# Kernel optimization log

Hardware: AMD Instinct MI355X
Metric: run time of the kernel (lower is better)

## Reference

```python
import jax, jax.numpy as jnp
import numpy as np
from jax import lax

FS, DW, CIN, COUT, NCLS, BATCH = 128, 8, 64, 256, 2, 512
K1, S1 = FS // 4, FS // 8          # 32, 16
L = FS * DW                        # 1024
T = (L - K1) // S1 + 1             # 63 SNN timesteps
BN_EPS = 1e-5


@jax.custom_vjp
def spike(u):
    """Heaviside spike on (v - threshold); surrogate grad exp(-|u|) (tau_grad=scale_grad=1)."""
    return (u >= 0).astype(u.dtype)

def _spike_fwd(u):
    return (u >= 0).astype(u.dtype), u

def _spike_bwd(u, g):
    return (g * jnp.exp(-jnp.abs(u)),)

spike.defvjp(_spike_fwd, _spike_bwd)


def cuba(x, threshold, current_decay, voltage_decay):
    """CUBA LIF scan. x: [N,C,T] -> binary spikes [N,C,T].
    i[t] = (1-cd)*i[t-1] + x[t]; v[t] = (1-vd)*v[t-1] + i[t]; s = v>=theta; v *= (1-s)."""
    cd, vd = 1.0 - current_decay, 1.0 - voltage_decay
    xs = jnp.moveaxis(x, -1, 0)  # [T,N,C]
    zero = jnp.zeros(x.shape[:-1], x.dtype)

    def step(carry, xt):
        i, v = carry
        i = cd * i + xt
        v = vd * v + i
        s = spike(v - threshold)
        v = v * (1.0 - s)
        return (i, v), s

    _, s = lax.scan(step, (zero, zero), xs)
    return jnp.moveaxis(s, 0, -1)


def conv1d(x, w, b, stride, pad):
    y = lax.conv_general_dilated(x, w, (stride,), [(pad, pad)],
                                 dimension_numbers=('NCH', 'OIH', 'NCH'))
    return y + b[None, :, None]


def bn(x, g, b, m, v):
    scale = g / jnp.sqrt(v + BN_EPS)
    return (x - m[None, :, None]) * scale[None, :, None] + b[None, :, None]


def setup_inputs() -> dict:
    key = jax.random.key(0)
    ks = jax.random.split(key, 12)
    return {
        'x':       jax.random.normal(ks[0], (BATCH, CIN, L), jnp.float32),
        'conv1_w': jax.random.normal(ks[1], (COUT, CIN, K1), jnp.float32) * 0.05,
        'conv1_b': jax.random.normal(ks[2], (COUT,), jnp.float32) * 0.05,
        'bn1_g':   jax.random.uniform(ks[3], (COUT,), jnp.float32, 0.5, 1.5),
        'bn1_b':   jax.random.normal(ks[4], (COUT,), jnp.float32) * 0.1,
        'bn1_m':   jax.random.normal(ks[5], (COUT,), jnp.float32) * 0.1,
        'bn1_v':   jax.random.uniform(ks[6], (COUT,), jnp.float32, 0.5, 1.5),
        'conv2_w': jax.random.normal(ks[7], (COUT, COUT, 3), jnp.float32) * 0.05,
        'conv2_b': jax.random.normal(ks[8], (COUT,), jnp.float32) * 0.05,
        'bn2_g':   jax.random.uniform(ks[9], (COUT,), jnp.float32, 0.5, 1.5),
        'bn2_b':   jax.random.normal(ks[10], (COUT,), jnp.float32) * 0.1,
        'bn2_m':   jax.random.normal(ks[11], (COUT,), jnp.float32) * 0.1,
        'bn2_v':   jax.random.uniform(jax.random.fold_in(key, 100), (COUT,), jnp.float32, 0.5, 1.5),
        'w1':      jax.random.normal(jax.random.fold_in(key, 101), (COUT, COUT), jnp.float32) * 0.1,
        'w2':      jax.random.normal(jax.random.fold_in(key, 102), (NCLS, COUT), jnp.float32) * 0.1,
    }


def reference(x, conv1_w, conv1_b, bn1_g, bn1_b, bn1_m, bn1_v,
              conv2_w, conv2_b, bn2_g, bn2_b, bn2_m, bn2_v, w1, w2):
    # CNN frontend (eval mode: BN uses running stats, dropout is identity)
    z = bn(conv1d(x, conv1_w, conv1_b, S1, 0), bn1_g, bn1_b, bn1_m, bn1_v)   # [N,COUT,T]
    z = bn(conv1d(z, conv2_w, conv2_b, 1, 1), bn2_g, bn2_b, bn2_m, bn2_v)    # [N,COUT,T]
    # CUBA Input encoder block: threshold=0.3, current_decay=0.9, voltage_decay=0.9
    z = cuba(z, 0.3, 0.9, 0.9)
    # CUBA Dense blocks (bias-free synapse per timestep + LIF): threshold=0.1, cd=1, vd=0.1
    z = cuba(jnp.einsum('oc,nct->not', w1, z), 0.1, 1.0, 0.1)
    z = cuba(jnp.einsum('oc,nct->not', w2, z), 0.1, 1.0, 0.1)
    return z  # binary spike trains [N, n_classes, T]
```

## Files before the change

### kernel.cpp

```cpp
#include <hip/hip_runtime.h>
#include <cstdint>
#include <cstddef>


typedef _Float16 half8 __attribute__((ext_vector_type(8)));
typedef float floatx4 __attribute__((ext_vector_type(4)));

__device__ __forceinline__ void split_f32(float v, _Float16& hi, _Float16& lo) {
    _Float16 h = (_Float16)v;
    hi = h;
    lo = (_Float16)((v - (float)h) * 2048.0f);
}

typedef const __attribute__((address_space(1))) unsigned int* gas_ptr;
typedef __attribute__((address_space(3))) unsigned int* las_ptr;
__device__ __forceinline__ void lds_dma16(const void* g, void* l) {
    __builtin_amdgcn_global_load_lds((gas_ptr)g, (las_ptr)l, 16, 0, 0);
}

__global__ __launch_bounds__(256) void prep_kernel(
    const float* __restrict__ c1w, const float* __restrict__ c1b,
    const float* __restrict__ g1,  const float* __restrict__ b1,
    const float* __restrict__ m1,  const float* __restrict__ v1,
    const float* __restrict__ c2w, const float* __restrict__ c2b,
    const float* __restrict__ g2,  const float* __restrict__ b2,
    const float* __restrict__ m2,  const float* __restrict__ v2,
    const float* __restrict__ w1,
    _Float16* __restrict__ w1h, _Float16* __restrict__ w1l,
    _Float16* __restrict__ w2h, _Float16* __restrict__ w2l,
    _Float16* __restrict__ wdh, _Float16* __restrict__ wdl,
    _Float16* __restrict__ z1ph, _Float16* __restrict__ z1pl,
    float* __restrict__ ab1, float* __restrict__ ab2)
{
    const int id = blockIdx.x * 256 + threadIdx.x;
    if (id < 256) {
        float a1 = g1[id] / sqrtf(v1[id] + 1e-5f);
        ab1[id]       = a1;
        ab1[256 + id] = (c1b[id] - m1[id]) * a1 + b1[id];
        float a2 = g2[id] / sqrtf(v2[id] + 1e-5f);
        ab2[id]       = a2;
        ab2[256 + id] = (c2b[id] - m2[id]) * a2 + b2[id];
    }
    {
        const int n  = id >> 7;
        const int j  = id & 127;
        const int row = (j < 64) ? 0 : 64;
        const int c0  = (j & 63) * 4;
        const size_t off = ((size_t)n * 65 + row) * 256 + c0;
        short4 zz = {0, 0, 0, 0};
        *(short4*)&z1ph[off] = zz;
        *(short4*)&z1pl[off] = zz;
    }
    split_f32(w1[id], wdh[id], wdl[id]);
    for (int idx = id; idx < 256 * 2048; idx += 65536)
        split_f32(c1w[idx], w1h[idx], w1l[idx]);
    for (int idx = id; idx < 256 * 768; idx += 65536) {
        const int o  = idx / 768;
        const int r  = idx - o * 768;
        const int dt = r >> 8;
        const int c  = r & 255;
        split_f32(c2w[o * 768 + c * 3 + dt], w2h[idx], w2l[idx]);
    }
}

__global__ __launch_bounds__(256, 2) void conv1_mfma(
    const float* __restrict__ x,
    const _Float16* __restrict__ w1h, const _Float16* __restrict__ w1l,
    const float* __restrict__ ab,
    _Float16* __restrict__ z1ph, _Float16* __restrict__ z1pl)
{
    __shared__ _Float16 Ah[4][128][8];
    __shared__ _Float16 Al[4][128][8];
    __shared__ _Float16 Bh[4][128][8];
    __shared__ _Float16 Bl[4][128][8];

    const int tid = threadIdx.x;
    const int bm = blockIdx.x, bn = blockIdx.y;
    const int lr = tid & 127;
    const int h  = tid >> 7;

    const int am = bm * 128 + lr;
    const int an = am / 63, at = am - an * 63;
    const float*    arow  = x   + (size_t)an * 65536 + at * 16 + h * 16;
    const _Float16* bhrow = w1h + (size_t)(bn * 128 + lr) * 2048 + h * 16;
    const _Float16* blrow = w1l + (size_t)(bn * 128 + lr) * 2048 + h * 16;

    const int lane = tid & 63;
    const int wv   = tid >> 6;
    const int mw   = wv & 1, nw = wv >> 1;
    const int quad = lane >> 4;
    const int l15  = lane & 15;

    floatx4 accA[4][4] = {};
    floatx4 accB[4][4] = {};

    for (int it = 0; it < 64; ++it) {
        const float* ap = arow + it * 1024;
        float va[16];
        *(float4*)&va[0]  = *(const float4*)(ap);
        *(float4*)&va[4]  = *(const float4*)(ap + 4);
        *(float4*)&va[8]  = *(const float4*)(ap + 8);
        *(float4*)&va[12] = *(const float4*)(ap + 12);
        int4 bh0 = *(const int4*)(bhrow + it * 32);
        int4 bh1 = *(const int4*)(bhrow + it * 32 + 8);
        int4 bl0 = *(const int4*)(blrow + it * 32);
        int4 bl1 = *(const int4*)(blrow + it * 32 + 8);

        union U { _Float16 hf[8]; int4 v; };
        U c0h, c0l, c1h, c1l;
#pragma unroll
        for (int j = 0; j < 8; ++j) split_f32(va[j],     c0h.hf[j], c0l.hf[j]);
#pragma unroll
        for (int j = 0; j < 8; ++j) split_f32(va[8 + j], c1h.hf[j], c1l.hf[j]);

        __syncthreads();
        *(int4*)&Ah[2*h  ][lr][0] = c0h.v;
        *(int4*)&Ah[2*h+1][lr][0] = c1h.v;
        *(int4*)&Al[2*h  ][lr][0] = c0l.v;
        *(int4*)&Al[2*h+1][lr][0] = c1l.v;
        *(int4*)&Bh[2*h  ][lr][0] = bh0;
        *(int4*)&Bh[2*h+1][lr][0] = bh1;
        *(int4*)&Bl[2*h  ][lr][0] = bl0;
        *(int4*)&Bl[2*h+1][lr][0] = bl1;
        __syncthreads();

        half8 fah[4], fal[4], fbh[4], fbl[4];
#pragma unroll
        for (int t = 0; t < 4; ++t) {
            fah[t] = *(const half8*)&Ah[quad][mw*64 + t*16 + l15][0];
            fal[t] = *(const half8*)&Al[quad][mw*64 + t*16 + l15][0];
            fbh[t] = *(const half8*)&Bh[quad][nw*64 + t*16 + l15][0];
            fbl[t] = *(const half8*)&Bl[quad][nw*64 + t*16 + l15][0];
        }
#pragma unroll
        for (int ti = 0; ti < 4; ++ti)
#pragma unroll
            for (int tj = 0; tj < 4; ++tj) {
                accA[ti][tj] = __builtin_amdgcn_mfma_f32_16x16x32_f16(fah[ti], fbh[tj], accA[ti][tj], 0, 0, 0);
                accB[ti][tj] = __builtin_amdgcn_mfma_f32_16x16x32_f16(fah[ti], fbl[tj], accB[ti][tj], 0, 0, 0);
                accB[ti][tj] = __builtin_amdgcn_mfma_f32_16x16x32_f16(fal[ti], fbh[tj], accB[ti][tj], 0, 0, 0);
            }
    }

#pragma unroll
    for (int tj = 0; tj < 4; ++tj) {
        const int o = bn*128 + nw*64 + tj*16 + l15;
        const float alpha = ab[o], beta = ab[256 + o];
#pragma unroll
        for (int ti = 0; ti < 4; ++ti) {
            const int m0 = bm*128 + mw*64 + ti*16 + quad*4;
#pragma unroll
            for (int r = 0; r < 4; ++r) {
                float c = accA[ti][tj][r] + accB[ti][tj][r] * (1.0f/2048.0f);
                float z = c * alpha + beta;
                _Float16 zh, zl;
                split_f32(z, zh, zl);
                const int m  = m0 + r;
                const int a2 = m / 63;
                const int t2 = m - a2 * 63;
                const size_t off = ((size_t)a2 * 65 + t2 + 1) * 256 + o;
                z1ph[off] = zh;
                z1pl[off] = zl;
            }
        }
    }
}

__global__ __launch_bounds__(256, 2) void conv2_mfma(
    const _Float16* __restrict__ z1ph, const _Float16* __restrict__ z1pl,
    const _Float16* __restrict__ w2h, const _Float16* __restrict__ w2l,
    const float* __restrict__ ab, float* __restrict__ z2)
{
    __shared__ _Float16 Ah[8][128][8];
    __shared__ _Float16 Al[8][128][8];
    __shared__ _Float16 Bh[8][128][8];
    __shared__ _Float16 Bl[8][128][8];

    const int tid = threadIdx.x;
    const int bm = blockIdx.x, bn = blockIdx.y;
    const int lr = tid & 127;
    const int h  = tid >> 7;

    const int am = bm * 128 + lr;
    const int an = am / 63, at = am - an * 63;
    const _Float16* pAh = z1ph + (size_t)an * 16640 + at * 256 + h * 8;
    const _Float16* pAl = z1pl + (size_t)an * 16640 + at * 256 + h * 8;
    const _Float16* pBh = w2h + (size_t)(bn * 128 + lr) * 768 + h * 8;
    const _Float16* pBl = w2l + (size_t)(bn * 128 + lr) * 768 + h * 8;

    const int lane = tid & 63;
    const int wv   = tid >> 6;
    const int mw   = wv & 1, nw = wv >> 1;
    const int quad = lane >> 4;
    const int l15  = lane & 15;

    floatx4 accA[4][4] = {};
    floatx4 accB[4][4] = {};

    for (int it = 0; it < 12; ++it) {
        __syncthreads();
#pragma unroll
        for (int q = 0; q < 4; ++q) {
            lds_dma16(pAh + q * 16, &Ah[q*2 + h][lr][0]);
            lds_dma16(pAl + q * 16, &Al[q*2 + h][lr][0]);
            lds_dma16(pBh + q * 16, &Bh[q*2 + h][lr][0]);
            lds_dma16(pBl + q * 16, &Bl[q*2 + h][lr][0]);
        }
        __syncthreads();

#pragma unroll
        for (int ks = 0; ks < 2; ++ks) {
            half8 fah[4], fal[4], fbh[4], fbl[4];
#pragma unroll
            for (int t = 0; t < 4; ++t) {
                fah[t] = *(const half8*)&Ah[ks*4 + quad][mw*64 + t*16 + l15][0];
                fal[t] = *(const half8*)&Al[ks*4 + quad][mw*64 + t*16 + l15][0];
                fbh[t] = *(const half8*)&Bh[ks*4 + quad][nw*64 + t*16 + l15][0];
                fbl[t] = *(const half8*)&Bl[ks*4 + quad][nw*64 + t*16 + l15][0];
            }
#pragma unroll
            for (int ti = 0; ti < 4; ++ti)
#pragma unroll
                for (int tj = 0; tj < 4; ++tj) {
                    accA[ti][tj] = __builtin_amdgcn_mfma_f32_16x16x32_f16(fah[ti], fbh[tj], accA[ti][tj], 0, 0, 0);
                    accB[ti][tj] = __builtin_amdgcn_mfma_f32_16x16x32_f16(fah[ti], fbl[tj], accB[ti][tj], 0, 0, 0);
                    accB[ti][tj] = __builtin_amdgcn_mfma_f32_16x16x32_f16(fal[ti], fbh[tj], accB[ti][tj], 0, 0, 0);
                }
        }
        pAh += 64; pAl += 64; pBh += 64; pBl += 64;
    }

#pragma unroll
    for (int tj = 0; tj < 4; ++tj) {
        const int o = bn*128 + nw*64 + tj*16 + l15;
        const float alpha = ab[o], beta = ab[256 + o];
#pragma unroll
        for (int ti = 0; ti < 4; ++ti) {
            const int m0 = bm*128 + mw*64 + ti*16 + quad*4;
#pragma unroll
            for (int r = 0; r < 4; ++r) {
                float c = accA[ti][tj][r] + accB[ti][tj][r] * (1.0f/2048.0f);
                z2[(size_t)(m0 + r) * 256 + o] = c * alpha + beta;
            }
        }
    }
}

__global__ __launch_bounds__(256) void cuba1_kernel(
    const float* __restrict__ z2, _Float16* __restrict__ s1)
{
    const int n   = blockIdx.x;
    const int tid = threadIdx.x;
    const float* zrow = z2 + (size_t)n * 16128 + tid;
    _Float16*    srow = s1 + (size_t)n * 16128 + tid;
    float cur = 0.f, vol = 0.f;
    for (int tb = 0; tb < 63; tb += 9) {
        float xv[9];
#pragma unroll
        for (int j = 0; j < 9; ++j)
            xv[j] = zrow[(size_t)(tb + j) * 256];
#pragma unroll
        for (int j = 0; j < 9; ++j) {
            cur = 0.1f * cur + xv[j];
            vol = 0.1f * vol + cur;
            bool sp = (vol - 0.3f) >= 0.f;
            srow[(size_t)(tb + j) * 256] = sp ? (_Float16)1.0f : (_Float16)0.0f;
            if (sp) vol = 0.f;
        }
    }
}

__global__ __launch_bounds__(256, 2) void dense1_mfma(
    const _Float16* __restrict__ s1,
    const _Float16* __restrict__ wdh, const _Float16* __restrict__ wdl,
    float* __restrict__ y1)
{
    __shared__ _Float16 As[8][128][8];
    __shared__ _Float16 Bh[8][128][8];
    __shared__ _Float16 Bl[8][128][8];

    const int tid = threadIdx.x;
    const int bm = blockIdx.x, bn = blockIdx.y;
    const int lr = tid & 127;
    const int h  = tid >> 7;

    const _Float16* pA  = s1  + (size_t)(bm * 128 + lr) * 256 + h * 8;
    const _Float16* pBh = wdh + (size_t)(bn * 128 + lr) * 256 + h * 8;
    const _Float16* pBl = wdl + (size_t)(bn * 128 + lr) * 256 + h * 8;

    const int lane = tid & 63;
    const int wv   = tid >> 6;
    const int mw   = wv & 1, nw = wv >> 1;
    const int quad = lane >> 4;
    const int l15  = lane & 15;

    floatx4 accA[4][4] = {};
    floatx4 accB[4][4] = {};

    for (int it = 0; it < 4; ++it) {
        __syncthreads();
#pragma unroll
        for (int q = 0; q < 4; ++q) {
            lds_dma16(pA  + q * 16, &As[q*2 + h][lr][0]);
            lds_dma16(pBh + q * 16, &Bh[q*2 + h][lr][0]);
            lds_dma16(pBl + q * 16, &Bl[q*2 + h][lr][0]);
        }
        __syncthreads();

#pragma unroll
        for (int ks = 0; ks < 2; ++ks) {
            half8 fa[4], fbh[4], fbl[4];
#pragma unroll
            for (int t = 0; t < 4; ++t) {
                fa[t]  = *(const half8*)&As[ks*4 + quad][mw*64 + t*16 + l15][0];
                fbh[t] = *(const half8*)&Bh[ks*4 + quad][nw*64 + t*16 + l15][0];
                fbl[t] = *(const half8*)&Bl[ks*4 + quad][nw*64 + t*16 + l15][0];
            }
#pragma unroll
            for (int ti = 0; ti < 4; ++ti)
#pragma unroll
                for (int tj = 0; tj < 4; ++tj) {
                    accA[ti][tj] = __builtin_amdgcn_mfma_f32_16x16x32_f16(fa[ti], fbh[tj], accA[ti][tj], 0, 0, 0);
                    accB[ti][tj] = __builtin_amdgcn_mfma_f32_16x16x32_f16(fa[ti], fbl[tj], accB[ti][tj], 0, 0, 0);
                }
        }
        pA += 64; pBh += 64; pBl += 64;
    }

#pragma unroll
    for (int tj = 0; tj < 4; ++tj) {
        const int o = bn*128 + nw*64 + tj*16 + l15;
#pragma unroll
        for (int ti = 0; ti < 4; ++ti) {
            const int m0 = bm*128 + mw*64 + ti*16 + quad*4;
#pragma unroll
            for (int r = 0; r < 4; ++r)
                y1[(size_t)(m0 + r) * 256 + o] =
                    accA[ti][tj][r] + accB[ti][tj][r] * (1.0f/2048.0f);
        }
    }
}

__global__ __launch_bounds__(256) void snn_tail(
    const float* __restrict__ y1, const float* __restrict__ w2,
    float* __restrict__ out)
{
    __shared__ unsigned long long M2[256];
    __shared__ float Y[2 * 63];
    const int n   = blockIdx.x;
    const int tid = threadIdx.x;

    {
        const float* yrow = y1 + (size_t)n * 16128 + tid;
        float v = 0.f;
        unsigned long long mask2 = 0ull;
        for (int t = 0; t < 63; ++t) {
            float yv = yrow[(size_t)t * 256];
            v = 0.9f * v + yv;
            if ((v - 0.1f) >= 0.f) { mask2 |= (1ull << t); v = 0.f; }
        }
        M2[tid] = mask2;
    }
    __syncthreads();

    if (tid < 126) {
        const int cls = tid / 63;
        const int t   = tid - cls * 63;
        const float* wrow = w2 + cls * 256;
        float acc = 0.f;
#pragma unroll 4
        for (int o = 0; o < 256; ++o)
            acc += ((M2[o] >> t) & 1ull) ? wrow[o] : 0.f;
        Y[cls * 63 + t] = acc;
    }
    __syncthreads();
    if (tid < 2) {
        float v = 0.f;
        float* orow = out + (size_t)n * 126 + tid * 63;
        for (int t = 0; t < 63; ++t) {
            v = 0.9f * v + Y[tid * 63 + t];
            float u = v - 0.1f;
            float s = (u >= 0.f) ? 1.f : 0.f;
            orow[t] = s;
            v = (u >= 0.f) ? 0.f : v;
        }
    }
}

extern "C" void kernel_launch(void* const* d_in, const int* in_sizes, int n_in,
                              void* d_out, int out_size, void* d_ws, size_t ws_size,
                              hipStream_t stream)
{
    const float* x    = (const float*)d_in[0];
    const float* c1w  = (const float*)d_in[1];
    const float* c1b  = (const float*)d_in[2];
    const float* g1   = (const float*)d_in[3];
    const float* b1   = (const float*)d_in[4];
    const float* m1   = (const float*)d_in[5];
    const float* v1   = (const float*)d_in[6];
    const float* c2w  = (const float*)d_in[7];
    const float* c2b  = (const float*)d_in[8];
    const float* g2   = (const float*)d_in[9];
    const float* b2   = (const float*)d_in[10];
    const float* m2   = (const float*)d_in[11];
    const float* v2   = (const float*)d_in[12];
    const float* w1   = (const float*)d_in[13];
    const float* w2   = (const float*)d_in[14];
    float* out = (float*)d_out;

    float* ws = (float*)d_ws;
    _Float16* z1ph = (_Float16*)ws;
    _Float16* z1pl = (_Float16*)(ws + 4259840);
    float*    y1   = ws;
    float*    z2   = ws + 8519680;
    _Float16* s1   = (_Float16*)(ws + 16777216);
    float*    wsp  = ws + 20905984;
    _Float16* w1h = (_Float16*)wsp;
    _Float16* w1l = (_Float16*)(wsp + 262144);
    _Float16* w2h = (_Float16*)(wsp + 2*262144);
    _Float16* w2l = (_Float16*)(wsp + 2*262144 + 98304);
    _Float16* wdh = (_Float16*)(wsp + 2*262144 + 2*98304);
    _Float16* wdl = (_Float16*)(wsp + 2*262144 + 2*98304 + 32768);
    float*    ab1 = wsp + 2*262144 + 2*98304 + 2*32768;
    float*    ab2 = ab1 + 512;

    prep_kernel<<<256, 256, 0, stream>>>(c1w, c1b, g1, b1, m1, v1,
                                         c2w, c2b, g2, b2, m2, v2,
                                         w1, w1h, w1l, w2h, w2l, wdh, wdl,
                                         z1ph, z1pl, ab1, ab2);
    conv1_mfma<<<dim3(252, 2), 256, 0, stream>>>(x, w1h, w1l, ab1, z1ph, z1pl);
    conv2_mfma<<<dim3(252, 2), 256, 0, stream>>>(z1ph, z1pl, w2h, w2l, ab2, z2);
    cuba1_kernel<<<512, 256, 0, stream>>>(z2, s1);
    dense1_mfma<<<dim3(252, 2), 256, 0, stream>>>(s1, wdh, wdl, y1);
    snn_tail<<<512, 256, 0, stream>>>(y1, w2, out);
}
```

Before: 446.7 us.

## Fuse CUBA scans into conv2 and dense1 GEMM epilogues via LDS tiles

Conv2 and dense1 tiles are re-aligned so that each block covers two full samples (64 rows each, padded from 63). The first CUBA scan then runs in the conv2 epilogue, and the dense LIF scan runs in the dense1 epilogue, both reading accumulators staged through LDS. This removes the fp32 z2 and y1 round trips to global memory and the separate cuba1 kernel launch. The cost is about 1.6% wasted MFMA rows from the padding, a padded z1 layout of 66 rows per sample, and a serial 63-step scan running inside the GEMM blocks.

New measurement: 429.8 us. 3.8% less time.

```diff
diff --git a/kernel.cpp b/kernel.cpp
--- a/kernel.cpp
+++ b/kernel.cpp
@@ -42,14 +42,17 @@
         ab2[256 + id] = (c2b[id] - m2[id]) * a2 + b2[id];
     }
     {
-        const int n  = id >> 7;
-        const int j  = id & 127;
-        const int row = (j < 64) ? 0 : 64;
-        const int c0  = (j & 63) * 4;
-        const size_t off = ((size_t)n * 65 + row) * 256 + c0;
         short4 zz = {0, 0, 0, 0};
-        *(short4*)&z1ph[off] = zz;
-        *(short4*)&z1pl[off] = zz;
+        for (int idx = id; idx < 98304; idx += 65536) {
+            const int n = idx / 192;
+            const int r = idx - n * 192;
+            const int rs = r >> 6;
+            const int row = (rs == 0) ? 0 : (63 + rs);
+            const int c0 = (r & 63) * 4;
+            const size_t off = ((size_t)n * 66 + row) * 256 + c0;
+            *(short4*)&z1ph[off] = zz;
+            *(short4*)&z1pl[off] = zz;
+        }
     }
     split_f32(w1[id], wdh[id], wdl[id]);
     for (int idx = id; idx < 256 * 2048; idx += 65536)
@@ -158,7 +161,7 @@
                 const int m  = m0 + r;
                 const int a2 = m / 63;
                 const int t2 = m - a2 * 63;
-                const size_t off = ((size_t)a2 * 65 + t2 + 1) * 256 + o;
+                const size_t off = ((size_t)a2 * 66 + t2 + 1) * 256 + o;
                 z1ph[off] = zh;
                 z1pl[off] = zl;
             }
@@ -166,25 +169,26 @@
     }
 }
 
-__global__ __launch_bounds__(256, 2) void conv2_mfma(
+__global__ __launch_bounds__(256, 2) void conv2_cuba_mfma(
     const _Float16* __restrict__ z1ph, const _Float16* __restrict__ z1pl,
     const _Float16* __restrict__ w2h, const _Float16* __restrict__ w2l,
-    const float* __restrict__ ab, float* __restrict__ z2)
-{
-    __shared__ _Float16 Ah[8][128][8];
-    __shared__ _Float16 Al[8][128][8];
-    __shared__ _Float16 Bh[8][128][8];
-    __shared__ _Float16 Bl[8][128][8];
+    const float* __restrict__ ab, _Float16* __restrict__ s1)
+{
+    __shared__ _Float16 SMEM[32768];
+    _Float16 (*Ah)[128][8] = reinterpret_cast<_Float16(*)[128][8]>(SMEM);
+    _Float16 (*Al)[128][8] = reinterpret_cast<_Float16(*)[128][8]>(SMEM + 8192);
+    _Float16 (*Bh)[128][8] = reinterpret_cast<_Float16(*)[128][8]>(SMEM + 16384);
+    _Float16 (*Bl)[128][8] = reinterpret_cast<_Float16(*)[128][8]>(SMEM + 24576);
 
     const int tid = threadIdx.x;
     const int bm = blockIdx.x, bn = blockIdx.y;
     const int lr = tid & 127;
     const int h  = tid >> 7;
 
-    const int am = bm * 128 + lr;
-    const int an = am / 63, at = am - an * 63;
-    const _Float16* pAh = z1ph + (size_t)an * 16640 + at * 256 + h * 8;
-    const _Float16* pAl = z1pl + (size_t)an * 16640 + at * 256 + h * 8;
+    const int n0 = bm * 2;
+    const int an = lr >> 6, at = lr & 63;
+    const _Float16* pAh = z1ph + ((size_t)(n0 + an) * 66 + at) * 256 + h * 8;
+    const _Float16* pAl = z1pl + ((size_t)(n0 + an) * 66 + at) * 256 + h * 8;
     const _Float16* pBh = w2h + (size_t)(bn * 128 + lr) * 768 + h * 8;
     const _Float16* pBl = w2l + (size_t)(bn * 128 + lr) * 768 + h * 8;
 
@@ -230,61 +234,58 @@
         pAh += 64; pAl += 64; pBh += 64; pBl += 64;
     }
 
+    __syncthreads();
+    float* zt = (float*)SMEM;
 #pragma unroll
     for (int tj = 0; tj < 4; ++tj) {
-        const int o = bn*128 + nw*64 + tj*16 + l15;
+        const int cl = nw*64 + tj*16 + l15;
+        const int o  = bn*128 + cl;
         const float alpha = ab[o], beta = ab[256 + o];
 #pragma unroll
         for (int ti = 0; ti < 4; ++ti) {
-            const int m0 = bm*128 + mw*64 + ti*16 + quad*4;
+            const int m0 = mw*64 + ti*16 + quad*4;
 #pragma unroll
             for (int r = 0; r < 4; ++r) {
                 float c = accA[ti][tj][r] + accB[ti][tj][r] * (1.0f/2048.0f);
-                z2[(size_t)(m0 + r) * 256 + o] = c * alpha + beta;
+                zt[(m0 + r) * 128 + cl] = c * alpha + beta;
             }
         }
     }
-}
-
-__global__ __launch_bounds__(256) void cuba1_kernel(
-    const float* __restrict__ z2, _Float16* __restrict__ s1)
-{
-    const int n   = blockIdx.x;
-    const int tid = threadIdx.x;
-    const float* zrow = z2 + (size_t)n * 16128 + tid;
-    _Float16*    srow = s1 + (size_t)n * 16128 + tid;
+    __syncthreads();
+
+    const int nl   = tid >> 7;
+    const int cloc = tid & 127;
+    const int n    = n0 + nl;
+    _Float16* srow = s1 + (size_t)n * 16128 + bn*128 + cloc;
     float cur = 0.f, vol = 0.f;
-    for (int tb = 0; tb < 63; tb += 9) {
-        float xv[9];
-#pragma unroll
-        for (int j = 0; j < 9; ++j)
-            xv[j] = zrow[(size_t)(tb + j) * 256];
-#pragma unroll
-        for (int j = 0; j < 9; ++j) {
-            cur = 0.1f * cur + xv[j];
-            vol = 0.1f * vol + cur;
-            bool sp = (vol - 0.3f) >= 0.f;
-            srow[(size_t)(tb + j) * 256] = sp ? (_Float16)1.0f : (_Float16)0.0f;
-            if (sp) vol = 0.f;
-        }
-    }
-}
-
-__global__ __launch_bounds__(256, 2) void dense1_mfma(
+    for (int t = 0; t < 63; ++t) {
+        float xv = zt[(nl*64 + t) * 128 + cloc];
+        cur = 0.1f * cur + xv;
+        vol = 0.1f * vol + cur;
+        bool sp = (vol - 0.3f) >= 0.f;
+        srow[(size_t)t * 256] = sp ? (_Float16)1.0f : (_Float16)0.0f;
+        if (sp) vol = 0.f;
+    }
+}
+
+__global__ __launch_bounds__(256, 2) void dense1_mask_mfma(
     const _Float16* __restrict__ s1,
     const _Float16* __restrict__ wdh, const _Float16* __restrict__ wdl,
-    float* __restrict__ y1)
-{
-    __shared__ _Float16 As[8][128][8];
-    __shared__ _Float16 Bh[8][128][8];
-    __shared__ _Float16 Bl[8][128][8];
+    unsigned long long* __restrict__ M2g)
+{
+    __shared__ _Float16 SMEM[32768];
+    _Float16 (*As)[128][8] = reinterpret_cast<_Float16(*)[128][8]>(SMEM);
+    _Float16 (*Bh)[128][8] = reinterpret_cast<_Float16(*)[128][8]>(SMEM + 8192);
+    _Float16 (*Bl)[128][8] = reinterpret_cast<_Float16(*)[128][8]>(SMEM + 16384);
 
     const int tid = threadIdx.x;
     const int bm = blockIdx.x, bn = blockIdx.y;
     const int lr = tid & 127;
     const int h  = tid >> 7;
 
-    const _Float16* pA  = s1  + (size_t)(bm * 128 + lr) * 256 + h * 8;
+    const int n0 = bm * 2;
+    const int an = lr >> 6, at = lr & 63;
+    const _Float16* pA  = s1  + ((size_t)(n0 + an) * 63 + at) * 256 + h * 8;
     const _Float16* pBh = wdh + (size_t)(bn * 128 + lr) * 256 + h * 8;
     const _Float16* pBl = wdl + (size_t)(bn * 128 + lr) * 256 + h * 8;
 
@@ -327,22 +328,36 @@
         pA += 64; pBh += 64; pBl += 64;
     }
 
+    __syncthreads();
+    float* yt = (float*)SMEM;
 #pragma unroll
     for (int tj = 0; tj < 4; ++tj) {
-        const int o = bn*128 + nw*64 + tj*16 + l15;
+        const int cl = nw*64 + tj*16 + l15;
 #pragma unroll
         for (int ti = 0; ti < 4; ++ti) {
-            const int m0 = bm*128 + mw*64 + ti*16 + quad*4;
+            const int m0 = mw*64 + ti*16 + quad*4;
 #pragma unroll
             for (int r = 0; r < 4; ++r)
-                y1[(size_t)(m0 + r) * 256 + o] =
+                yt[(m0 + r) * 128 + cl] =
                     accA[ti][tj][r] + accB[ti][tj][r] * (1.0f/2048.0f);
         }
     }
+    __syncthreads();
+
+    const int nl   = tid >> 7;
+    const int oloc = tid & 127;
+    unsigned long long mask = 0ull;
+    float v = 0.f;
+    for (int t = 0; t < 63; ++t) {
+        float yv = yt[(nl*64 + t) * 128 + oloc];
+        v = 0.9f * v + yv;
+        if ((v - 0.1f) >= 0.f) { mask |= (1ull << t); v = 0.f; }
+    }
+    M2g[(size_t)(n0 + nl) * 256 + bn*128 + oloc] = mask;
 }
 
 __global__ __launch_bounds__(256) void snn_tail(
-    const float* __restrict__ y1, const float* __restrict__ w2,
+    const unsigned long long* __restrict__ M2g, const float* __restrict__ w2,
     float* __restrict__ out)
 {
     __shared__ unsigned long long M2[256];
@@ -350,17 +365,7 @@
     const int n   = blockIdx.x;
     const int tid = threadIdx.x;
 
-    {
-        const float* yrow = y1 + (size_t)n * 16128 + tid;
-        float v = 0.f;
-        unsigned long long mask2 = 0ull;
-        for (int t = 0; t < 63; ++t) {
-            float yv = yrow[(size_t)t * 256];
-            v = 0.9f * v + yv;
-            if ((v - 0.1f) >= 0.f) { mask2 |= (1ull << t); v = 0.f; }
-        }
-        M2[tid] = mask2;
-    }
+    M2[tid] = M2g[(size_t)n * 256 + tid];
     __syncthreads();
 
     if (tid < 126) {
@@ -410,11 +415,10 @@
 
     float* ws = (float*)d_ws;
     _Float16* z1ph = (_Float16*)ws;
-    _Float16* z1pl = (_Float16*)(ws + 4259840);
-    float*    y1   = ws;
-    float*    z2   = ws + 8519680;
-    _Float16* s1   = (_Float16*)(ws + 16777216);
-    float*    wsp  = ws + 20905984;
+    _Float16* z1pl = (_Float16*)(ws + 4325376);
+    _Float16* s1   = (_Float16*)(ws + 8650752);
+    unsigned long long* M2g = (unsigned long long*)(ws + 12779520);
+    float*    wsp  = ws + 13041664;
     _Float16* w1h = (_Float16*)wsp;
     _Float16* w1l = (_Float16*)(wsp + 262144);
     _Float16* w2h = (_Float16*)(wsp + 2*262144);
@@ -429,8 +433,7 @@
                                          w1, w1h, w1l, w2h, w2l, wdh, wdl,
                                          z1ph, z1pl, ab1, ab2);
     conv1_mfma<<<dim3(252, 2), 256, 0, stream>>>(x, w1h, w1l, ab1, z1ph, z1pl);
-    conv2_mfma<<<dim3(252, 2), 256, 0, stream>>>(z1ph, z1pl, w2h, w2l, ab2, z2);
-    cuba1_kernel<<<512, 256, 0, stream>>>(z2, s1);
-    dense1_mfma<<<dim3(252, 2), 256, 0, stream>>>(s1, wdh, wdl, y1);
-    snn_tail<<<512, 256, 0, stream>>>(y1, w2, out);
-}
+    conv2_cuba_mfma<<<dim3(256, 2), 256, 0, stream>>>(z1ph, z1pl, w2h, w2l, ab2, s1);
+    dense1_mask_mfma<<<dim3(256, 2), 256, 0, stream>>>(s1, wdh, wdl, M2g);
+    snn_tail<<<512, 256, 0, stream>>>(M2g, w2, out);
+}
```
